# Kernel tuning notes

Hardware: AMD Instinct MI355X
Metric: run time of the kernel (lower is better)

## Reference

```python
import jax, jax.numpy as jnp
import numpy as np

B, N, D, H = 4, 2048, 64, 8

def setup_inputs() -> dict:
    key = jax.random.key(0)
    ks = jax.random.split(key, 6)
    s = 0.05
    return {
        "x":  jax.random.normal(ks[0], (B, N, D), dtype=jnp.float32),
        "Wq": jax.random.normal(ks[1], (D, D * H), dtype=jnp.float32) * s,
        "Wk": jax.random.normal(ks[2], (D, D * H), dtype=jnp.float32) * s,
        "Wv": jax.random.normal(ks[3], (D, D * H), dtype=jnp.float32) * s,
        "Wu": jax.random.normal(ks[4], (D * H, D), dtype=jnp.float32) * s,
        "bu": jnp.zeros((D,), dtype=jnp.float32),
    }

def reference(x, Wq, Wk, Wv, Wu, bu):
    b, n, d = x.shape
    h = Wq.shape[1] // d
    # projections: each head has full width d (per the original module)
    q = (x @ Wq).reshape(b, n, h, d).transpose(0, 2, 1, 3)  # [b,h,n,d]
    k = (x @ Wk).reshape(b, n, h, d).transpose(0, 2, 1, 3)
    v = (x @ Wv).reshape(b, n, h, d).transpose(0, 2, 1, 3)
    scores = jnp.einsum('bhnd,bhmd->bhnm', q, k) / jnp.sqrt(jnp.float32(d))
    w = jax.nn.softmax(scores, axis=-1)
    y = jnp.einsum('bhnm,bhmd->bhnd', w, v)          # [b,h,n,d]
    y = y.transpose(0, 2, 1, 3).reshape(b, n, h * d)  # [b,n,h*d]
    return y @ Wu + bu
```

## Files before the change

### kernel.cpp

```cpp
#include <hip/hip_runtime.h>
#include <hip/hip_bf16.h>

#define BB 4
#define NN 2048
#define DD 64
#define HH 8
#define DHH 512

typedef __bf16 bf16_t;
typedef __bf16 bf16x8 __attribute__((ext_vector_type(8)));
typedef __bf16 bf16x4 __attribute__((ext_vector_type(4)));
typedef float f32x4 __attribute__((ext_vector_type(4)));
typedef long long i64;
typedef i64 i64x2 __attribute__((ext_vector_type(2)));
typedef _Float16 f16_t;
typedef _Float16 f16x4 __attribute__((ext_vector_type(4)));
typedef __fp16 h16x2 __attribute__((ext_vector_type(2)));

__device__ __forceinline__ void dma16(const void* g, void* l) {
    __builtin_amdgcn_global_load_lds(
        (const __attribute__((address_space(1))) unsigned int*)g,
        (__attribute__((address_space(3))) unsigned int*)l,
        16, 0, 0);
}

#define MFMA   __builtin_amdgcn_mfma_f32_16x16x32_bf16
#define MFMA8  __builtin_amdgcn_mfma_f32_16x16x32_fp8_fp8
#define MFMA16F __builtin_amdgcn_mfma_f32_16x16x16f16

#define QSCALE 0.18033688011112042f


__global__ __launch_bounds__(256) void prep(
    const float* __restrict__ Wq, const float* __restrict__ Wk,
    const float* __restrict__ Wv, const float* __restrict__ Wu,
    bf16_t* __restrict__ Wqt, bf16_t* __restrict__ Wkt,
    bf16_t* __restrict__ Wvt, bf16_t* __restrict__ Wut)
{
    const int bid = blockIdx.x, tid = threadIdx.x;
    if (bid < 12) {
        const int m = bid >> 2, slice = bid & 3;
        const float* src = (m == 0) ? Wq : (m == 1) ? Wk : Wv;
        bf16_t* dst = (m == 0) ? Wqt : (m == 1) ? Wkt : Wvt;
        const float scale = (m == 0) ? QSCALE : 1.0f;
        const int dc = slice * 128 + (tid >> 1);
        const int kbase = (tid & 1) * 32;
        #pragma unroll
        for (int k0 = 0; k0 < 4; ++k0) {
            bf16x8 p;
            #pragma unroll
            for (int j = 0; j < 8; ++j)
                p[j] = (bf16_t)(src[(size_t)(kbase + k0 * 8 + j) * 512 + dc] * scale);
            *(bf16x8*)(dst + dc * 64 + kbase + k0 * 8) = p;
        }
    } else {
        const int kq = (bid - 12) * 128;
        const int dc = tid >> 2, sub = (tid & 3) * 32;
        #pragma unroll
        for (int k0 = 0; k0 < 4; ++k0) {
            bf16x8 p;
            #pragma unroll
            for (int j = 0; j < 8; ++j)
                p[j] = (bf16_t)Wu[(size_t)(kq + sub + k0 * 8 + j) * 64 + dc];
            *(bf16x8*)(Wut + dc * 512 + kq + sub + k0 * 8) = p;
        }
    }
}

__global__ __launch_bounds__(256) void qkv_mfma(
    const float* __restrict__ x, const bf16_t* __restrict__ Wqt,
    const bf16_t* __restrict__ Wkt, const bf16_t* __restrict__ Wvt,
    char* __restrict__ q8, char* __restrict__ k8, f16_t* __restrict__ vt)
{
    const int n0   = blockIdx.x * 64;
    const int h    = blockIdx.y;
    const int tid  = threadIdx.x;
    const int w    = tid >> 6;
    const int lane = tid & 63;
    const int quad = lane >> 4;
    const int c    = lane & 15;
    const int cq   = c & 7;
    const int l8   = lane >> 3;
    const int lg   = (lane & 7) ^ l8;
    const int lo   = l8 * 128 + lg * 16;
    const int sw0  = ((quad    ) ^ cq) * 16;
    const int sw1  = ((quad + 4) ^ cq) * 16;
    const int w2048 = w * 2048;

    __shared__ __align__(16) float  xs[64 * 64];
    __shared__ __align__(16) bf16_t Wqs[64 * 64], Wks[64 * 64], Wvs[64 * 64];

    {
        const int rloc = lane >> 4;
        const int s    = lane & 15;
        #pragma unroll
        for (int j = 0; j < 4; ++j) {
            int chunk = w * 4 + j;
            int r7 = (chunk * 4 + rloc) & 7;
            const char* src = (const char*)(x + (size_t)(n0 + chunk * 4 + rloc) * 64)
                            + ((s & 8) | ((s & 7) ^ r7)) * 16;
            dma16(src, (char*)xs + chunk * 1024);
        }
    }
    const char* qg = (const char*)Wqt + (size_t)h * 8192;
    const char* kg = (const char*)Wkt + (size_t)h * 8192;
    const char* vg = (const char*)Wvt + (size_t)h * 8192;
    dma16(qg + w2048 + lo,        (char*)Wqs + w2048);
    dma16(qg + w2048 + 1024 + lo, (char*)Wqs + w2048 + 1024);
    dma16(kg + w2048 + lo,        (char*)Wks + w2048);
    dma16(kg + w2048 + 1024 + lo, (char*)Wks + w2048 + 1024);
    dma16(vg + w2048 + lo,        (char*)Wvs + w2048);
    dma16(vg + w2048 + 1024 + lo, (char*)Wvs + w2048 + 1024);
    __syncthreads();

    auto xfrag = [&](int row, int kk) -> bf16x8 {
        const char* rbase = (const char*)xs + row * 256;
        int g0 = kk * 8 + ((quad * 2    ) ^ cq);
        int g1 = kk * 8 + ((quad * 2 + 1) ^ cq);
        f32x4 a = *(const f32x4*)(rbase + g0 * 16);
        f32x4 b = *(const f32x4*)(rbase + g1 * 16);
        bf16x8 r;
        r[0] = (bf16_t)a[0]; r[1] = (bf16_t)a[1]; r[2] = (bf16_t)a[2]; r[3] = (bf16_t)a[3];
        r[4] = (bf16_t)b[0]; r[5] = (bf16_t)b[1]; r[6] = (bf16_t)b[2]; r[7] = (bf16_t)b[3];
        return r;
    };

    bf16x8 xf0 = xfrag(w * 16 + c, 0);
    bf16x8 xf1 = xfrag(w * 16 + c, 1);

    const int gr = n0 + w * 16 + c;
    const int bb = gr >> 11, nn = gr & 2047;
    char* qrow_g = q8 + (((size_t)bb * HH + h) * NN + nn) * 64;
    char* krow_g = k8 + (((size_t)bb * HH + h) * NN + nn) * 64;
    const int nsw = (nn & 3) ^ ((nn >> 2) & 3);

    #pragma unroll
    for (int mb = 0; mb < 4; ++mb) {
        const char* aq = (const char*)Wqs + (mb * 16 + c) * 128;
        const char* ak = (const char*)Wks + (mb * 16 + c) * 128;
        f32x4 accq = (f32x4){0.f, 0.f, 0.f, 0.f};
        f32x4 acck = (f32x4){0.f, 0.f, 0.f, 0.f};
        accq = MFMA(*(const bf16x8*)(aq + sw0), xf0, accq, 0, 0, 0);
        accq = MFMA(*(const bf16x8*)(aq + sw1), xf1, accq, 0, 0, 0);
        acck = MFMA(*(const bf16x8*)(ak + sw0), xf0, acck, 0, 0, 0);
        acck = MFMA(*(const bf16x8*)(ak + sw1), xf1, acck, 0, 0, 0);
        int g2  = (mb * 2 + (quad >> 1)) & 3;
        int off = ((quad & 1) * 4) + ((mb >> 1) * 8) + ((g2 ^ nsw) * 16);
        int pq = __builtin_amdgcn_cvt_pk_fp8_f32(accq[0], accq[1], 0, false);
        pq     = __builtin_amdgcn_cvt_pk_fp8_f32(accq[2], accq[3], pq, true);
        int pk = __builtin_amdgcn_cvt_pk_fp8_f32(acck[0], acck[1], 0, false);
        pk     = __builtin_amdgcn_cvt_pk_fp8_f32(acck[2], acck[3], pk, true);
        *(int*)(qrow_g + off) = pq;
        *(int*)(krow_g + off) = pk;
    }

    const char* wvrow = (const char*)Wvs + (w * 16 + c) * 128;
    bf16x8 vf0 = *(const bf16x8*)(wvrow + sw0);
    bf16x8 vf1 = *(const bf16x8*)(wvrow + sw1);

    const int bb2 = n0 >> 11;
    f16_t* vtb = vt + ((size_t)bb2 * HH + h) * (size_t)(DD * NN)
               + (size_t)((n0 & 2047) >> 4) * 1024 + (w * 16 + c) * 16 + quad * 4;

    #pragma unroll
    for (int nb = 0; nb < 4; ++nb) {
        f32x4 acc = (f32x4){0.f, 0.f, 0.f, 0.f};
        acc = MFMA(xfrag(nb * 16 + c, 0), vf0, acc, 0, 0, 0);
        acc = MFMA(xfrag(nb * 16 + c, 1), vf1, acc, 0, 0, 0);
        f16x4 p = { (f16_t)acc[0], (f16_t)acc[1], (f16_t)acc[2], (f16_t)acc[3] };
        *(f16x4*)(vtb + nb * 1024) = p;
    }
}

__global__ __launch_bounds__(256, 3) void flash_attn(
    const char* __restrict__ q8, const char* __restrict__ k8,
    const f16_t* __restrict__ vt, bf16_t* __restrict__ y)
{
    const int h    = blockIdx.x;
    const int n0   = blockIdx.y * 64;
    const int b    = blockIdx.z;
    const int tid  = threadIdx.x;
    const int w    = tid >> 6;
    const int lane = tid & 63;
    const int quad = lane >> 4;
    const int c    = lane & 15;
    const int ksw  = (quad ^ (c & 3) ^ ((c >> 2) & 3)) * 16;

    __shared__ __align__(16) char SM[17408];

    const size_t bh = (size_t)(b * HH + h);
    const char* qp = q8 + bh * (size_t)(NN * 64);
    const char* kp = k8 + bh * (size_t)(NN * 64);
    const char* vp = (const char*)(vt + bh * (size_t)(DD * NN));

    i64x2 qf[4];
    #pragma unroll
    for (int cb = 0; cb < 4; ++cb)
        qf[cb] = *(const i64x2*)(qp + (size_t)(n0 + cb * 16 + c) * 64 + ksw);

    const char* kglob = kp + w * 1024 + (size_t)c * 64 + ksw;
    const char* vglob = vp + w * 2048 + (size_t)c * 32 + quad * 8;

    f32x4 lsum4[4];
    f32x4 o[4][4];
    #pragma unroll
    for (int cb = 0; cb < 4; ++cb) lsum4[cb] = (f32x4){0.f, 0.f, 0.f, 0.f};
    #pragma unroll
    for (int db = 0; db < 4; ++db)
        #pragma unroll
        for (int cb = 0; cb < 4; ++cb) o[db][cb] = (f32x4){0.f, 0.f, 0.f, 0.f};

    #define LOADT(kf_, vf_, t) do {                                         \
        const char* kg_ = kglob + (size_t)(t) * 4096;                       \
        const char* vg_ = vglob + (size_t)(t) * 8192;                       \
        kf_     = *(const i64x2*)(kg_);                                     \
        vf_[0]  = *(const f16x4*)(vg_);                                     \
        vf_[1]  = *(const f16x4*)(vg_ + 512);                               \
        vf_[2]  = *(const f16x4*)(vg_ + 1024);                              \
        vf_[3]  = *(const f16x4*)(vg_ + 1536);                              \
    } while (0)

    #define BODYR(kf_, vf_) do {                                            \
        _Pragma("unroll")                                                   \
        for (int cb = 0; cb < 4; ++cb) {                                    \
            f32x4 s_ = (f32x4){0.f, 0.f, 0.f, 0.f};                         \
            s_ = MFMA8(kf_.x, qf[cb].x, s_, 0, 0, 0);                       \
            s_ = MFMA8(kf_.y, qf[cb].y, s_, 0, 0, 0);                       \
            float p0_ = __builtin_amdgcn_exp2f(s_[0]);                      \
            float p1_ = __builtin_amdgcn_exp2f(s_[1]);                      \
            float p2_ = __builtin_amdgcn_exp2f(s_[2]);                      \
            float p3_ = __builtin_amdgcn_exp2f(s_[3]);                      \
            lsum4[cb] += (f32x4){p0_, p1_, p2_, p3_};                       \
            h16x2 ab_ = __builtin_amdgcn_cvt_pkrtz(p0_, p1_);               \
            h16x2 cd_ = __builtin_amdgcn_cvt_pkrtz(p2_, p3_);               \
            f16x4 pf_;                                                      \
            __builtin_memcpy(&pf_, &ab_, 4);                                \
            __builtin_memcpy((char*)&pf_ + 4, &cd_, 4);                     \
            _Pragma("unroll")                                               \
            for (int db = 0; db < 4; ++db)                                  \
                o[db][cb] = MFMA16F(vf_[db], pf_, o[db][cb], 0, 0, 0);      \
        }                                                                   \
    } while (0)

    i64x2 kA, kB, kC;
    f16x4 vA[4], vB[4], vC[4];
    LOADT(kA, vA, 0);
    LOADT(kB, vB, 1);
    LOADT(kC, vC, 2);

    #pragma unroll 1
    for (int j = 0; j < 10; ++j) {
        const int t = j * 3;
        const int ta = (t + 3 < 32) ? t + 3 : 31;
        const int tb = (t + 4 < 32) ? t + 4 : 31;
        const int tc = (t + 5 < 32) ? t + 5 : 31;
        BODYR(kA, vA); LOADT(kA, vA, ta);
        BODYR(kB, vB); LOADT(kB, vB, tb);
        BODYR(kC, vC); LOADT(kC, vC, tc);
    }
    BODYR(kA, vA);
    BODYR(kB, vB);

    #undef LOADT
    #undef BODYR

    float lsum[4];
    #pragma unroll
    for (int cb = 0; cb < 4; ++cb)
        lsum[cb] = (lsum4[cb][0] + lsum4[cb][1]) + (lsum4[cb][2] + lsum4[cb][3]);

    char*  Ob = SM;
    float* Lb = (float*)(SM + 16384);

    #pragma unroll
    for (int cb = 0; cb < 4; ++cb) {
        lsum[cb] += __shfl_xor(lsum[cb], 16, 64);
        lsum[cb] += __shfl_xor(lsum[cb], 32, 64);
    }
    if (quad == 0) {
        #pragma unroll
        for (int cb = 0; cb < 4; ++cb)
            Lb[(w * 4 + cb) * 16 + c] = lsum[cb];
    }

    #pragma unroll
    for (int ww = 0; ww < 4; ++ww) {
        if (w == ww) {
            #pragma unroll
            for (int db = 0; db < 4; ++db) {
                #pragma unroll
                for (int cb = 0; cb < 4; ++cb) {
                    char* p = Ob + (size_t)(((db * 4 + cb) * 4 + quad) * 16 + c) * 16;
                    f32x4 v = o[db][cb];
                    if (ww > 0) v += *(const f32x4*)p;
                    *(f32x4*)p = v;
                }
            }
        }
        __syncthreads();
    }

    {
        const int n_loc = tid & 63;
        const int dq    = tid >> 6;
        const int qcb   = n_loc >> 4;
        const int cc    = n_loc & 15;
        float l = Lb[(0 * 4 + qcb) * 16 + cc] + Lb[(1 * 4 + qcb) * 16 + cc]
                + Lb[(2 * 4 + qcb) * 16 + cc] + Lb[(3 * 4 + qcb) * 16 + cc];
        float inv = 1.0f / l;
        float vals[16];
        #pragma unroll
        for (int q2 = 0; q2 < 4; ++q2) {
            f32x4 v = *(const f32x4*)(Ob
                    + (size_t)(((dq * 4 + qcb) * 4 + q2) * 16 + cc) * 16);
            vals[q2 * 4 + 0] = v[0]; vals[q2 * 4 + 1] = v[1];
            vals[q2 * 4 + 2] = v[2]; vals[q2 * 4 + 3] = v[3];
        }
        bf16x8 o0, o1;
        #pragma unroll
        for (int j = 0; j < 8; ++j) {
            o0[j] = (bf16_t)(vals[j] * inv);
            o1[j] = (bf16_t)(vals[8 + j] * inv);
        }
        bf16_t* yrow = y + bh * (size_t)(NN * DD) + (size_t)(n0 + n_loc) * DD + dq * 16;
        *(bf16x8*)(yrow)     = o0;
        *(bf16x8*)(yrow + 8) = o1;
    }
}

__global__ __launch_bounds__(256) void out_proj(
    const bf16_t* __restrict__ y,
    const bf16_t* __restrict__ Wut,
    const float* __restrict__ bu, float* __restrict__ out)
{
    const int rt   = blockIdx.x >> 1;
    const int dh   = blockIdx.x & 1;
    const int row0 = rt * 32;
    const int b    = row0 >> 11;
    const int nn0  = row0 & 2047;
    const int tid  = threadIdx.x;
    const int w    = tid >> 6;
    const int lane = tid & 63;
    const int quad = lane >> 4;
    const int c    = lane & 15;
    const int cq   = c & 7;

    __shared__ __align__(16) bf16_t ys[32 * 512];

    {
        const int hsel = lane >> 3;
        const int g7   = lane & 7;
        #pragma unroll
        for (int rr = 0; rr < 8; ++rr) {
            int row = w * 8 + rr;
            const char* src = (const char*)y
                + (((size_t)b * HH + hsel) * NN + nn0 + row) * 128
                + ((g7 ^ (row & 7)) * 16);
            dma16(src, (char*)ys + row * 1024);
        }
    }
    __syncthreads();

    const int rows16 = (w >> 1) * 16;
    const int mb     = dh * 2 + (w & 1);
    const char* yrow = (const char*)ys + (rows16 + c) * 1024;

    f32x4 acc = (f32x4){0.f, 0.f, 0.f, 0.f};
    #pragma unroll
    for (int kk = 0; kk < 16; ++kk) {
        int g = kk * 4 + quad;
        bf16x8 bfrag = *(const bf16x8*)(yrow + (((g & ~7) | ((g & 7) ^ cq)) * 16));
        bf16x8 afrag = *(const bf16x8*)((const char*)Wut
                        + (size_t)(mb * 16 + c) * 1024 + kk * 64 + quad * 16);
        acc = MFMA(afrag, bfrag, acc, 0, 0, 0);
    }

    float4 bb = *(const float4*)(bu + mb * 16 + quad * 4);
    float4 res = { acc[0] + bb.x, acc[1] + bb.y, acc[2] + bb.z, acc[3] + bb.w };
    float* op = out + (size_t)(row0 + rows16 + c) * DD + mb * 16 + quad * 4;
    *(float4*)op = res;
}

extern "C" void kernel_launch(void* const* d_in, const int* in_sizes, int n_in,
                              void* d_out, int out_size, void* d_ws, size_t ws_size,
                              hipStream_t stream) {
    const float* x  = (const float*)d_in[0];
    const float* Wq = (const float*)d_in[1];
    const float* Wk = (const float*)d_in[2];
    const float* Wv = (const float*)d_in[3];
    const float* Wu = (const float*)d_in[4];
    const float* bu = (const float*)d_in[5];
    float* out = (float*)d_out;

    const size_t SEG8 = (size_t)BB * HH * NN * 64;
    const size_t SEG  = SEG8 * 2;
    char* ws = (char*)d_ws;
    char*   q8  = ws;
    char*   k8  = ws + SEG8;
    f16_t*  vt  = (f16_t*)(ws + 2 * SEG8);
    bf16_t* y   = (bf16_t*)(ws + 2 * SEG8 + SEG);
    bf16_t* Wqt = (bf16_t*)(ws + 2 * SEG8 + 2 * SEG);
    bf16_t* Wkt = (bf16_t*)(ws + 2 * SEG8 + 2 * SEG + (1 << 16));
    bf16_t* Wvt = (bf16_t*)(ws + 2 * SEG8 + 2 * SEG + 2 * (1 << 16));
    bf16_t* Wut = (bf16_t*)(ws + 2 * SEG8 + 2 * SEG + 3 * (1 << 16));

    prep<<<dim3(16), dim3(256), 0, stream>>>(Wq, Wk, Wv, Wu, Wqt, Wkt, Wvt, Wut);
    qkv_mfma<<<dim3(128, 8), dim3(256), 0, stream>>>(x, Wqt, Wkt, Wvt, q8, k8, vt);
    flash_attn<<<dim3(HH, NN / 64, BB), dim3(256), 0, stream>>>(q8, k8, vt, y);
    out_proj<<<dim3(512), dim3(256), 0, stream>>>(y, Wut, bu, out);
}
```

Measured before the change: 141.7 us.

## Stage K/V tiles through double-buffered LDS using async global_load_lds DMA

The attention loop used to prefetch K and V fragments straight into registers, three tiles ahead. It now copies pairs of K/V tiles into a double-buffered 48KB shared-memory region with global_load_lds. Each tile is read back from LDS with the old swizzled addressing, and a barrier separates the stages. The V-transpose write layout in the projection kernel changes to match the contiguous DMA copy. The aim is to drop register pressure from the prefetch and overlap memory with compute. In exchange it adds per-step barriers and LDS round trips, and the larger LDS footprint may limit occupancy.

```diff
diff --git a/kernel.cpp b/kernel.cpp
--- a/kernel.cpp
+++ b/kernel.cpp
@@ -160,7 +160,7 @@
 
     const int bb2 = n0 >> 11;
     f16_t* vtb = vt + ((size_t)bb2 * HH + h) * (size_t)(DD * NN)
-               + (size_t)((n0 & 2047) >> 4) * 1024 + (w * 16 + c) * 16 + quad * 4;
+               + (size_t)((n0 & 2047) >> 4) * 1024 + quad * 256 + (w * 16 + c) * 4;
 
     #pragma unroll
     for (int nb = 0; nb < 4; ++nb) {
@@ -186,7 +186,7 @@
     const int c    = lane & 15;
     const int ksw  = (quad ^ (c & 3) ^ ((c >> 2) & 3)) * 16;
 
-    __shared__ __align__(16) char SM[17408];
+    __shared__ __align__(16) char SM[49152];
 
     const size_t bh = (size_t)(b * HH + h);
     const char* qp = q8 + bh * (size_t)(NN * 64);
@@ -198,8 +198,11 @@
     for (int cb = 0; cb < 4; ++cb)
         qf[cb] = *(const i64x2*)(qp + (size_t)(n0 + cb * 16 + c) * 64 + ksw);
 
-    const char* kglob = kp + w * 1024 + (size_t)c * 64 + ksw;
-    const char* vglob = vp + w * 2048 + (size_t)c * 32 + quad * 8;
+    const char* kdma = kp + w * 1024 + lane * 16;
+    const char* vdma = vp + w * 2048 + lane * 16;
+
+    const int kro = w * 2048 + c * 64 + ksw;
+    const int vro = 8192 + w * 4096 + quad * 512 + c * 8;
 
     f32x4 lsum4[4];
     f32x4 o[4][4];
@@ -210,64 +213,68 @@
         #pragma unroll
         for (int cb = 0; cb < 4; ++cb) o[db][cb] = (f32x4){0.f, 0.f, 0.f, 0.f};
 
-    #define LOADT(kf_, vf_, t) do {                                         \
-        const char* kg_ = kglob + (size_t)(t) * 4096;                       \
-        const char* vg_ = vglob + (size_t)(t) * 8192;                       \
-        kf_     = *(const i64x2*)(kg_);                                     \
-        vf_[0]  = *(const f16x4*)(vg_);                                     \
-        vf_[1]  = *(const f16x4*)(vg_ + 512);                               \
-        vf_[2]  = *(const f16x4*)(vg_ + 1024);                              \
-        vf_[3]  = *(const f16x4*)(vg_ + 1536);                              \
+    #define STAGE2(p, buf) do {                                               \
+        char* B_ = SM + (buf) * 24576;                                        \
+        const size_t t0_ = (size_t)(2 * (p));                                 \
+        dma16(kdma + t0_ * 4096,         B_ + w * 2048);                      \
+        dma16(kdma + t0_ * 4096 + 4096,  B_ + w * 2048 + 1024);               \
+        dma16(vdma + t0_ * 8192,         B_ + 8192 + w * 4096);               \
+        dma16(vdma + t0_ * 8192 + 1024,  B_ + 8192 + w * 4096 + 1024);        \
+        dma16(vdma + t0_ * 8192 + 8192,  B_ + 8192 + w * 4096 + 2048);        \
+        dma16(vdma + t0_ * 8192 + 9216,  B_ + 8192 + w * 4096 + 3072);        \
     } while (0)
 
-    #define BODYR(kf_, vf_) do {                                            \
-        _Pragma("unroll")                                                   \
-        for (int cb = 0; cb < 4; ++cb) {                                    \
-            f32x4 s_ = (f32x4){0.f, 0.f, 0.f, 0.f};                         \
-            s_ = MFMA8(kf_.x, qf[cb].x, s_, 0, 0, 0);                       \
-            s_ = MFMA8(kf_.y, qf[cb].y, s_, 0, 0, 0);                       \
-            float p0_ = __builtin_amdgcn_exp2f(s_[0]);                      \
-            float p1_ = __builtin_amdgcn_exp2f(s_[1]);                      \
-            float p2_ = __builtin_amdgcn_exp2f(s_[2]);                      \
-            float p3_ = __builtin_amdgcn_exp2f(s_[3]);                      \
-            lsum4[cb] += (f32x4){p0_, p1_, p2_, p3_};                       \
-            h16x2 ab_ = __builtin_amdgcn_cvt_pkrtz(p0_, p1_);               \
-            h16x2 cd_ = __builtin_amdgcn_cvt_pkrtz(p2_, p3_);               \
-            f16x4 pf_;                                                      \
-            __builtin_memcpy(&pf_, &ab_, 4);                                \
-            __builtin_memcpy((char*)&pf_ + 4, &cd_, 4);                     \
-            _Pragma("unroll")                                               \
-            for (int db = 0; db < 4; ++db)                                  \
-                o[db][cb] = MFMA16F(vf_[db], pf_, o[db][cb], 0, 0, 0);      \
-        }                                                                   \
+    #define BODY2(buf, hf) do {                                               \
+        const char* kb_b = SM + (buf) * 24576;                                \
+        i64x2 kf_ = *(const i64x2*)(kb_b + kro + (hf) * 1024);                \
+        f16x4 vf_[4];                                                         \
+        _Pragma("unroll")                                                     \
+        for (int db = 0; db < 4; ++db)                                        \
+            vf_[db] = *(const f16x4*)(kb_b + vro + (hf) * 2048 + db * 128);   \
+        _Pragma("unroll")                                                     \
+        for (int cb = 0; cb < 4; ++cb) {                                      \
+            f32x4 s_ = (f32x4){0.f, 0.f, 0.f, 0.f};                           \
+            s_ = MFMA8(kf_.x, qf[cb].x, s_, 0, 0, 0);                         \
+            s_ = MFMA8(kf_.y, qf[cb].y, s_, 0, 0, 0);                         \
+            float p0_ = __builtin_amdgcn_exp2f(s_[0]);                        \
+            float p1_ = __builtin_amdgcn_exp2f(s_[1]);                        \
+            float p2_ = __builtin_amdgcn_exp2f(s_[2]);                        \
+            float p3_ = __builtin_amdgcn_exp2f(s_[3]);                        \
+            lsum4[cb] += (f32x4){p0_, p1_, p2_, p3_};                         \
+            h16x2 ab_ = __builtin_amdgcn_cvt_pkrtz(p0_, p1_);                 \
+            h16x2 cd_ = __builtin_amdgcn_cvt_pkrtz(p2_, p3_);                 \
+            f16x4 pf_;                                                        \
+            __builtin_memcpy(&pf_, &ab_, 4);                                  \
+            __builtin_memcpy((char*)&pf_ + 4, &cd_, 4);                       \
+            _Pragma("unroll")                                                 \
+            for (int db = 0; db < 4; ++db)                                    \
+                o[db][cb] = MFMA16F(vf_[db], pf_, o[db][cb], 0, 0, 0);        \
+        }                                                                     \
     } while (0)
 
-    i64x2 kA, kB, kC;
-    f16x4 vA[4], vB[4], vC[4];
-    LOADT(kA, vA, 0);
-    LOADT(kB, vB, 1);
-    LOADT(kC, vC, 2);
+    STAGE2(0, 0);
+    __syncthreads();
+    STAGE2(1, 1);
 
     #pragma unroll 1
-    for (int j = 0; j < 10; ++j) {
-        const int t = j * 3;
-        const int ta = (t + 3 < 32) ? t + 3 : 31;
-        const int tb = (t + 4 < 32) ? t + 4 : 31;
-        const int tc = (t + 5 < 32) ? t + 5 : 31;
-        BODYR(kA, vA); LOADT(kA, vA, ta);
-        BODYR(kB, vB); LOADT(kB, vB, tb);
-        BODYR(kC, vC); LOADT(kC, vC, tc);
-    }
-    BODYR(kA, vA);
-    BODYR(kB, vB);
-
-    #undef LOADT
-    #undef BODYR
+    for (int p = 0; p < 16; ++p) {
+        if (p > 0) {
+            __syncthreads();
+            if (p < 15) STAGE2(p + 1, (p + 1) & 1);
+        }
+        BODY2(p & 1, 0);
+        BODY2(p & 1, 1);
+    }
+
+    #undef STAGE2
+    #undef BODY2
 
     float lsum[4];
     #pragma unroll
     for (int cb = 0; cb < 4; ++cb)
         lsum[cb] = (lsum4[cb][0] + lsum4[cb][1]) + (lsum4[cb][2] + lsum4[cb][3]);
+
+    __syncthreads();
 
     char*  Ob = SM;
     float* Lb = (float*)(SM + 16384);
```

New measurement: 128.1 us. -9.6%, faster.
